# Optimization experiments

Measured on AMD Instinct MI355X. Metric: run time of the kernel, lower is better.

The kernel has to match this reference:

```python
import jax, jax.numpy as jnp
import numpy as np


def setup_inputs() -> dict:
    key = jax.random.key(0)
    k1, k2 = jax.random.split(key)
    S_src, S_tgt, B, H = 2048, 2048, 16, 256
    out_e = jax.random.normal(k1, (S_src, B, 2 * H), dtype=jnp.float32)
    out_d = jax.random.normal(k2, (S_tgt, B, H), dtype=jnp.float32)
    return {"out_e": out_e, "out_d": out_d}


def reference(out_e, out_d):
    # out_e: [S_src, B, 2*H] (bidirectional), out_d: [S_tgt, B, H]
    S, B, H2 = out_e.shape
    # sum the two directions: [S, B, H]
    enc = out_e.reshape(S, B, 2, H2 // 2).sum(axis=2)
    enc = enc.transpose(1, 0, 2)   # [B, S_src, H]
    dec = out_d.transpose(1, 0, 2)  # [B, S_tgt, H]
    # attn scores [B, S_src, S_tgt]; softmax over source positions (dim=1)
    attn = jnp.einsum('bsh,bth->bst', enc, dec)
    attn = jax.nn.softmax(attn, axis=1)
    # context: weighted sum over source positions -> [B, S_tgt, H]
    context = jnp.einsum('bst,bsh->bth', attn, enc)
    return context.transpose(1, 0, 2)  # [S_tgt, B, H]
```

## Files before the change

kernel.cpp:

```cpp
#include <hip/hip_runtime.h>
#include <stdint.h>
#include <stddef.h>

#define BATCH 16
#define SEQ 2048
#define HDIM 256
#define SCHUNK 32
#define TTILE 128
#define NCHUNK 64
#define TILE_U16 8192
#define NTILES 1024
#define PREBLK 2048
#define KSTRIDE 260

typedef float f32x4 __attribute__((ext_vector_type(4)));
typedef float f32x16 __attribute__((ext_vector_type(16)));
typedef _Float16 f16x8 __attribute__((ext_vector_type(8)));
typedef __bf16 bf16x8 __attribute__((ext_vector_type(8)));
typedef unsigned short u16;
typedef u16 u16x8 __attribute__((ext_vector_type(8)));
typedef unsigned int u32;
typedef u32 u32x4 __attribute__((ext_vector_type(4)));
typedef const __attribute__((address_space(1))) u32* gp1_t;
typedef __attribute__((address_space(3))) u32* lp3_t;

static __device__ __forceinline__ u16 f2bf(float f) {
  union { float f; unsigned int u; } v; v.f = f;
  unsigned int u = v.u;
  unsigned int r = u + 0x7FFFu + ((u >> 16) & 1u);
  return (u16)(r >> 16);
}

__global__ __launch_bounds__(256, 8)
void prepass_kernel(const float* __restrict__ e,
                    u16* __restrict__ KH, u16* __restrict__ VT) {
  __shared__ float Ks[16 * KSTRIDE];
  const int tid = threadIdx.x;
  const int bid = blockIdx.x;
  const int h2  = bid & 1;
  const int tb  = bid >> 1;
  const int b   = tb >> 6;
  const int ck  = tb & 63;
  const size_t tile = (size_t)tb * TILE_U16;
  const int r0 = h2 * 16;

  {
    int row = tid >> 4;
    int c16 = tid & 15;
    const float* src = e + ((size_t)(ck * SCHUNK + r0 + row) * BATCH + b) * (2 * HDIM);
#pragma unroll
    for (int u = 0; u < 4; ++u) {
      int col = c16 * 4 + 64 * u;
      float4 xa = *(const float4*)(src + col);
      float4 xb = *(const float4*)(src + col + HDIM);
      float4 s; s.x = xa.x + xb.x; s.y = xa.y + xb.y; s.z = xa.z + xb.z; s.w = xa.w + xb.w;
      *(float4*)&Ks[row * KSTRIDE + col] = s;
    }
  }
  __syncthreads();

  const int lane = tid & 63;
  const int w = tid >> 6;

  {
    int half = lane >> 5;
    int l5   = lane & 31;
    int lm   = l5 & 15;
    int g    = (l5 >> 4) & 1;
#pragma unroll
    for (int i = 0; i < 2; ++i) {
      int kb = w * 4 + i * 2 + half;
      const float* rp = &Ks[lm * KSTRIDE + kb * 16 + g * 8];
      u16x8 hi;
#pragma unroll
      for (int j = 0; j < 8; ++j)
        hi[j] = __builtin_bit_cast(u16, (_Float16)rp[j]);
      int lane_out = g * 32 + r0 + lm;
      *(u16x8*)&KH[tile + (size_t)(kb * 64 + lane_out) * 8] = hi;
    }
  }

  {
    int m = lane & 31;
    int g = lane >> 5;
#pragma unroll
    for (int i = 0; i < 2; ++i) {
      int ht = w * 2 + i;
      int fr = ht * 2 + h2;
      u16x8 v;
#pragma unroll
      for (int j = 0; j < 8; ++j)
        v[j] = f2bf(Ks[(g * 8 + j) * KSTRIDE + ht * 32 + m]);
      *(u16x8*)&VT[tile + (size_t)(fr * 64 + lane) * 8] = v;
    }
  }
}

__global__ __launch_bounds__(512, 2)
void attn_main_kernel(const u16* __restrict__ KH, const u16* __restrict__ VT,
                      const float* __restrict__ dq,
                      float* __restrict__ out) {
  __shared__ alignas(16) u16 KHs[4][TILE_U16];
  __shared__ alignas(16) u16 VTs[6][TILE_U16];

  const int tid  = threadIdx.x;
  const int lane = tid & 63;
  const int wv   = tid >> 6;
  const int wq   = wv & 3;
  const int grp  = wv >> 2;
  const int m    = lane & 31;
  const int g    = lane >> 5;

  const int bid = blockIdx.x;
  const int b  = ((bid & 7) << 1) | ((bid >> 3) & 1);
  const int t0 = (bid >> 4) * TTILE;

  const int tq = t0 + wq * 32 + m;
  const float* qp = dq + ((size_t)tq * BATCH + b) * HDIM;
  f16x8 qh[16];
#pragma unroll
  for (int kb = 0; kb < 16; ++kb) {
    int h = kb * 16 + g * 8;
    float4 f0 = *(const float4*)(qp + h);
    float4 f1 = *(const float4*)(qp + h + 4);
    float xs[8] = {f0.x, f0.y, f0.z, f0.w, f1.x, f1.y, f1.z, f1.w};
    u16x8 hb;
#pragma unroll
    for (int j = 0; j < 8; ++j)
      hb[j] = __builtin_bit_cast(u16, (_Float16)xs[j]);
    qh[kb] = __builtin_bit_cast(f16x8, hb);
  }

  f32x16 ctx[8];
#pragma unroll
  for (int ht = 0; ht < 8; ++ht) ctx[ht] = (f32x16)(0.0f);
  float dsum = 0.0f;
  bf16x8 pa0 = {}, pa1 = {};

  const bool isVT  = (wv >> 1) & 1;
  const int  choff = wv >> 2;
  const int  subbase = (wv & 1) * 8;
  const u16* srcArr = isVT ? VT : KH;
  auto stage = [&](int p) {
    int ckk = 2 * p + choff;
    int ktile = 2 * (p & 1) + choff;
    int vtile = (p % 3) * 2 + choff;
    size_t tb = ((size_t)b * NCHUNK + ckk) * TILE_U16;
    u16* dst = isVT ? &VTs[vtile][0] : &KHs[ktile][0];
#pragma unroll
    for (int i = 0; i < 8; ++i) {
      int sub = subbase + i;
      __builtin_amdgcn_global_load_lds(
          (gp1_t)(const void*)&srcArr[tb + (size_t)sub * 512 + lane * 8],
          (lp3_t)(void*)&dst[sub * 512], 16, 0, 0);
    }
  };

  auto qk = [&](int p, f32x16& a0, f32x16& a1) {
    int kt = 2 * (p & 1) + grp;
#pragma unroll
    for (int kb = 0; kb < 16; kb += 2) {
      f16x8 k0 = __builtin_bit_cast(f16x8, *(const u16x8*)&KHs[kt][kb * 512 + lane * 8]);
      f16x8 k1 = __builtin_bit_cast(f16x8, *(const u16x8*)&KHs[kt][(kb + 1) * 512 + lane * 8]);
      a0 = __builtin_amdgcn_mfma_f32_32x32x16_f16(k0, qh[kb], a0, 0, 0, 0);
      a1 = __builtin_amdgcn_mfma_f32_32x32x16_f16(k1, qh[kb + 1], a1, 0, 0, 0);
    }
  };

  auto pv = [&](int p) {
    int vt_ = (p % 3) * 2 + grp;
#pragma unroll
    for (int ht = 0; ht < 8; ++ht) {
      bf16x8 v0 = __builtin_bit_cast(bf16x8, *(const u16x8*)&VTs[vt_][(ht * 2) * 512 + lane * 8]);
      bf16x8 v1 = __builtin_bit_cast(bf16x8, *(const u16x8*)&VTs[vt_][(ht * 2 + 1) * 512 + lane * 8]);
      ctx[ht] = __builtin_amdgcn_mfma_f32_32x32x16_bf16(pa0, v0, ctx[ht], 0, 0, 0);
      ctx[ht] = __builtin_amdgcn_mfma_f32_32x32x16_bf16(pa1, v1, ctx[ht], 0, 0, 0);
    }
  };

  auto softmax_pack = [&](const f32x16& a0, const f32x16& a1) {
    float pf[16];
#pragma unroll
    for (int r = 0; r < 16; ++r) {
      pf[r] = __expf(a0[r] + a1[r] - 128.0f);
      dsum += pf[r];
    }
    u32 c[8];
#pragma unroll
    for (int q = 0; q < 8; ++q)
      asm("v_cvt_pk_bf16_f32 %0, %1, %2"
          : "=v"(c[q]) : "v"(pf[2 * q]), "v"(pf[2 * q + 1]));
    asm("v_permlane32_swap_b32 %0, %1" : "+v"(c[0]), "+v"(c[2]));
    asm("v_permlane32_swap_b32 %0, %1" : "+v"(c[1]), "+v"(c[3]));
    asm("v_permlane32_swap_b32 %0, %1" : "+v"(c[4]), "+v"(c[6]));
    asm("v_permlane32_swap_b32 %0, %1" : "+v"(c[5]), "+v"(c[7]));
    u32x4 w0 = {c[0], c[1], c[2], c[3]};
    u32x4 w1 = {c[4], c[5], c[6], c[7]};
    pa0 = __builtin_bit_cast(bf16x8, w0);
    pa1 = __builtin_bit_cast(bf16x8, w1);
  };

  stage(0);
  stage(1);
  asm volatile("s_waitcnt vmcnt(8)" ::: "memory");
  __builtin_amdgcn_s_barrier();
  {
    f32x16 a0 = (f32x16)(0.0f), a1 = (f32x16)(0.0f);
    qk(0, a0, a1);
    softmax_pack(a0, a1);
  }

  for (int j = 0; j < 32; ++j) {
    asm volatile("s_waitcnt vmcnt(0)" ::: "memory");
    __builtin_amdgcn_s_barrier();
    if (j < 30) stage(j + 2);

    f32x16 a0 = (f32x16)(0.0f), a1 = (f32x16)(0.0f);
    __builtin_amdgcn_s_setprio(1);
    if (j < 31) qk(j + 1, a0, a1);
    pv(j);
    __builtin_amdgcn_s_setprio(0);
    if (j < 31) softmax_pack(a0, a1);
  }

  dsum += __shfl_xor(dsum, 32, 64);
  __syncthreads();

  float* exch = (wq == 0) ? (float*)&KHs[0][0]
              : (wq == 1) ? (float*)&KHs[2][0]
              : (wq == 2) ? (float*)&VTs[0][0]
                          : (float*)&VTs[2][0];
  float* dex = (float*)&VTs[4][0];

  if (grp == 1) {
#pragma unroll
    for (int r4 = 0; r4 < 4; ++r4)
#pragma unroll
      for (int ht = 0; ht < 8; ++ht) {
        f32x4 v = {ctx[ht][r4 * 4], ctx[ht][r4 * 4 + 1],
                   ctx[ht][r4 * 4 + 2], ctx[ht][r4 * 4 + 3]};
        *(f32x4*)&exch[r4 * 2048 + ht * 256 + lane * 4] = v;
      }
    dex[wq * 64 + lane] = dsum;
  }
  __syncthreads();

  if (grp == 0) {
    float dB = dex[wq * 64 + lane];
    float inv = 1.0f / (dsum + dB);
#pragma unroll
    for (int r4 = 0; r4 < 4; ++r4)
#pragma unroll
      for (int ht = 0; ht < 8; ++ht) {
        f32x4 v = *(const f32x4*)&exch[r4 * 2048 + ht * 256 + lane * 4];
        ctx[ht][r4 * 4]     += v[0];
        ctx[ht][r4 * 4 + 1] += v[1];
        ctx[ht][r4 * 4 + 2] += v[2];
        ctx[ht][r4 * 4 + 3] += v[3];
      }
#pragma unroll
    for (int r = 0; r < 16; ++r) {
      int tl = (r & 3) + 8 * (r >> 2) + 4 * g;
      float rinv = __shfl(inv, tl, 64);
      int t = t0 + wq * 32 + tl;
      float* op = out + ((size_t)t * BATCH + b) * HDIM + m;
#pragma unroll
      for (int ht = 0; ht < 8; ++ht)
        op[ht * 32] = ctx[ht][r] * rinv;
    }
  }
}

extern "C" void kernel_launch(void* const* d_in, const int* in_sizes, int n_in,
                              void* d_out, int out_size, void* d_ws, size_t ws_size,
                              hipStream_t stream) {
  const float* e  = (const float*)d_in[0];
  const float* dq = (const float*)d_in[1];
  float* out = (float*)d_out;
  u16* KH = (u16*)d_ws;
  u16* VT = KH + (size_t)NTILES * TILE_U16;
  prepass_kernel<<<dim3(PREBLK), dim3(256), 0, stream>>>(e, KH, VT);
  attn_main_kernel<<<dim3(BATCH * (SEQ / TTILE)), dim3(512), 0, stream>>>(
      KH, VT, dq, out);
}
```

Measured before the change: 200.8 us.

## Load V tiles directly from global into registers instead of staging in LDS

Removes the six-slot LDS ring for V tiles. Each wave now loads its V fragments straight from global memory into registers, software-pipelined two steps ahead inside the PV MFMA loop. Only K tiles stay staged in LDS, and the staging work is spread over all eight waves. This cuts LDS use a lot, which may allow more blocks per CU and removes LDS write/read traffic for V. The cost is global-load latency on the PV path, since each V tile is now read separately by waves of different blocks. The context reduction is split into two phases so it fits the smaller shared buffer.

```diff
diff --git a/kernel.cpp b/kernel.cpp
--- a/kernel.cpp
+++ b/kernel.cpp
@@ -101,7 +101,7 @@
                       const float* __restrict__ dq,
                       float* __restrict__ out) {
   __shared__ alignas(16) u16 KHs[4][TILE_U16];
-  __shared__ alignas(16) u16 VTs[6][TILE_U16];
+  __shared__ float dex[256];
 
   const int tid  = threadIdx.x;
   const int lane = tid & 63;
@@ -137,21 +137,16 @@
   float dsum = 0.0f;
   bf16x8 pa0 = {}, pa1 = {};
 
-  const bool isVT  = (wv >> 1) & 1;
-  const int  choff = wv >> 2;
-  const int  subbase = (wv & 1) * 8;
-  const u16* srcArr = isVT ? VT : KH;
   auto stage = [&](int p) {
-    int ckk = 2 * p + choff;
-    int ktile = 2 * (p & 1) + choff;
-    int vtile = (p % 3) * 2 + choff;
-    size_t tb = ((size_t)b * NCHUNK + ckk) * TILE_U16;
-    u16* dst = isVT ? &VTs[vtile][0] : &KHs[ktile][0];
-#pragma unroll
-    for (int i = 0; i < 8; ++i) {
-      int sub = subbase + i;
+    int ck2   = 2 * p + (wv >> 2);
+    int ktile = 2 * (p & 1) + (wv >> 2);
+    size_t tb = ((size_t)b * NCHUNK + ck2) * TILE_U16;
+    u16* dst = &KHs[ktile][0];
+#pragma unroll
+    for (int i = 0; i < 4; ++i) {
+      int sub = (wv & 3) * 4 + i;
       __builtin_amdgcn_global_load_lds(
-          (gp1_t)(const void*)&srcArr[tb + (size_t)sub * 512 + lane * 8],
+          (gp1_t)(const void*)&KH[tb + (size_t)sub * 512 + lane * 8],
           (lp3_t)(void*)&dst[sub * 512], 16, 0, 0);
     }
   };
@@ -164,17 +159,6 @@
       f16x8 k1 = __builtin_bit_cast(f16x8, *(const u16x8*)&KHs[kt][(kb + 1) * 512 + lane * 8]);
       a0 = __builtin_amdgcn_mfma_f32_32x32x16_f16(k0, qh[kb], a0, 0, 0, 0);
       a1 = __builtin_amdgcn_mfma_f32_32x32x16_f16(k1, qh[kb + 1], a1, 0, 0, 0);
-    }
-  };
-
-  auto pv = [&](int p) {
-    int vt_ = (p % 3) * 2 + grp;
-#pragma unroll
-    for (int ht = 0; ht < 8; ++ht) {
-      bf16x8 v0 = __builtin_bit_cast(bf16x8, *(const u16x8*)&VTs[vt_][(ht * 2) * 512 + lane * 8]);
-      bf16x8 v1 = __builtin_bit_cast(bf16x8, *(const u16x8*)&VTs[vt_][(ht * 2 + 1) * 512 + lane * 8]);
-      ctx[ht] = __builtin_amdgcn_mfma_f32_32x32x16_bf16(pa0, v0, ctx[ht], 0, 0, 0);
-      ctx[ht] = __builtin_amdgcn_mfma_f32_32x32x16_bf16(pa1, v1, ctx[ht], 0, 0, 0);
     }
   };
 
@@ -202,7 +186,7 @@
 
   stage(0);
   stage(1);
-  asm volatile("s_waitcnt vmcnt(8)" ::: "memory");
+  asm volatile("s_waitcnt vmcnt(4)" ::: "memory");
   __builtin_amdgcn_s_barrier();
   {
     f32x16 a0 = (f32x16)(0.0f), a1 = (f32x16)(0.0f);
@@ -213,61 +197,89 @@
   for (int j = 0; j < 32; ++j) {
     asm volatile("s_waitcnt vmcnt(0)" ::: "memory");
     __builtin_amdgcn_s_barrier();
+
+    const int ckk = 2 * j + grp;
+    const u16* vb = VT + ((size_t)b * NCHUNK + ckk) * TILE_U16;
+
+    u16x8 vv0[8], vv1[8];
+    vv0[0] = *(const u16x8*)&vb[(size_t)(0 * 64 + lane) * 8];
+    vv1[0] = *(const u16x8*)&vb[(size_t)(1 * 64 + lane) * 8];
+    vv0[1] = *(const u16x8*)&vb[(size_t)(2 * 64 + lane) * 8];
+    vv1[1] = *(const u16x8*)&vb[(size_t)(3 * 64 + lane) * 8];
+
     if (j < 30) stage(j + 2);
 
     f32x16 a0 = (f32x16)(0.0f), a1 = (f32x16)(0.0f);
     __builtin_amdgcn_s_setprio(1);
     if (j < 31) qk(j + 1, a0, a1);
-    pv(j);
+
+#pragma unroll
+    for (int ht = 0; ht < 8; ++ht) {
+      if (ht < 6) {
+        vv0[ht + 2] = *(const u16x8*)&vb[(size_t)((2 * ht + 4) * 64 + lane) * 8];
+        vv1[ht + 2] = *(const u16x8*)&vb[(size_t)((2 * ht + 5) * 64 + lane) * 8];
+      }
+      bf16x8 v0 = __builtin_bit_cast(bf16x8, vv0[ht]);
+      bf16x8 v1 = __builtin_bit_cast(bf16x8, vv1[ht]);
+      ctx[ht] = __builtin_amdgcn_mfma_f32_32x32x16_bf16(pa0, v0, ctx[ht], 0, 0, 0);
+      ctx[ht] = __builtin_amdgcn_mfma_f32_32x32x16_bf16(pa1, v1, ctx[ht], 0, 0, 0);
+    }
     __builtin_amdgcn_s_setprio(0);
+
     if (j < 31) softmax_pack(a0, a1);
   }
 
   dsum += __shfl_xor(dsum, 32, 64);
   __syncthreads();
 
-  float* exch = (wq == 0) ? (float*)&KHs[0][0]
-              : (wq == 1) ? (float*)&KHs[2][0]
-              : (wq == 2) ? (float*)&VTs[0][0]
-                          : (float*)&VTs[2][0];
-  float* dex = (float*)&VTs[4][0];
-
-  if (grp == 1) {
-#pragma unroll
-    for (int r4 = 0; r4 < 4; ++r4)
-#pragma unroll
-      for (int ht = 0; ht < 8; ++ht) {
-        f32x4 v = {ctx[ht][r4 * 4], ctx[ht][r4 * 4 + 1],
-                   ctx[ht][r4 * 4 + 2], ctx[ht][r4 * 4 + 3]};
-        *(f32x4*)&exch[r4 * 2048 + ht * 256 + lane * 4] = v;
+  float* exch = (float*)&KHs[0][0] + wq * 4096;
+  float inv = 0.0f;
+
+#pragma unroll
+  for (int ph = 0; ph < 2; ++ph) {
+    if (grp == 1) {
+#pragma unroll
+      for (int r4 = 0; r4 < 4; ++r4)
+#pragma unroll
+        for (int hh = 0; hh < 4; ++hh) {
+          int ht = ph * 4 + hh;
+          f32x4 v = {ctx[ht][r4 * 4], ctx[ht][r4 * 4 + 1],
+                     ctx[ht][r4 * 4 + 2], ctx[ht][r4 * 4 + 3]};
+          *(f32x4*)&exch[r4 * 1024 + hh * 256 + lane * 4] = v;
+        }
+      if (ph == 0) dex[wq * 64 + lane] = dsum;
+    }
+    __syncthreads();
+    if (grp == 0) {
+      if (ph == 0) {
+        float dB = dex[wq * 64 + lane];
+        inv = 1.0f / (dsum + dB);
       }
-    dex[wq * 64 + lane] = dsum;
-  }
-  __syncthreads();
-
-  if (grp == 0) {
-    float dB = dex[wq * 64 + lane];
-    float inv = 1.0f / (dsum + dB);
-#pragma unroll
-    for (int r4 = 0; r4 < 4; ++r4)
-#pragma unroll
-      for (int ht = 0; ht < 8; ++ht) {
-        f32x4 v = *(const f32x4*)&exch[r4 * 2048 + ht * 256 + lane * 4];
-        ctx[ht][r4 * 4]     += v[0];
-        ctx[ht][r4 * 4 + 1] += v[1];
-        ctx[ht][r4 * 4 + 2] += v[2];
-        ctx[ht][r4 * 4 + 3] += v[3];
+#pragma unroll
+      for (int r4 = 0; r4 < 4; ++r4)
+#pragma unroll
+        for (int hh = 0; hh < 4; ++hh) {
+          int ht = ph * 4 + hh;
+          f32x4 v = *(const f32x4*)&exch[r4 * 1024 + hh * 256 + lane * 4];
+          ctx[ht][r4 * 4]     += v[0];
+          ctx[ht][r4 * 4 + 1] += v[1];
+          ctx[ht][r4 * 4 + 2] += v[2];
+          ctx[ht][r4 * 4 + 3] += v[3];
+        }
+#pragma unroll
+      for (int r = 0; r < 16; ++r) {
+        int tl = (r & 3) + 8 * (r >> 2) + 4 * g;
+        float rinv = __shfl(inv, tl, 64);
+        int t = t0 + wq * 32 + tl;
+        float* op = out + ((size_t)t * BATCH + b) * HDIM + m;
+#pragma unroll
+        for (int hh = 0; hh < 4; ++hh) {
+          int ht = ph * 4 + hh;
+          op[ht * 32] = ctx[ht][r] * rinv;
+        }
       }
-#pragma unroll
-    for (int r = 0; r < 16; ++r) {
-      int tl = (r & 3) + 8 * (r >> 2) + 4 * g;
-      float rinv = __shfl(inv, tl, 64);
-      int t = t0 + wq * 32 + tl;
-      float* op = out + ((size_t)t * BATCH + b) * HDIM + m;
-#pragma unroll
-      for (int ht = 0; ht < 8; ++ht)
-        op[ht * 32] = ctx[ht][r] * rinv;
-    }
+    }
+    __syncthreads();
   }
 }
 
```

Result: slower. 298.8 us (+48.8%).

## Split source chunks across blocks with atomic reduction instead of intra-block wave groups

Applied to the files above, without the earlier changes.

Replaces the 512-thread block, whose two wave groups split the source chunks and reduce through LDS, with 256-thread blocks that each handle half the source range. This doubles the grid, halves LDS use per block and should allow more resident blocks. Partial context and denominators are combined with global float atomicAdds into the zeroed output and a global denominator array, then a separate divide kernel normalises. The cost is two extra kernel launches, an extra pass over the output, atomic traffic, and a summation order that is no longer deterministic.

```diff
diff --git a/kernel.cpp b/kernel.cpp
--- a/kernel.cpp
+++ b/kernel.cpp
@@ -24,11 +24,21 @@
 typedef const __attribute__((address_space(1))) u32* gp1_t;
 typedef __attribute__((address_space(3))) u32* lp3_t;
 
+__device__ alignas(16) float g_den[SEQ * BATCH];
+
 static __device__ __forceinline__ u16 f2bf(float f) {
   union { float f; unsigned int u; } v; v.f = f;
   unsigned int u = v.u;
   unsigned int r = u + 0x7FFFu + ((u >> 16) & 1u);
   return (u16)(r >> 16);
+}
+
+__global__ __launch_bounds__(256, 8)
+void zero_kernel(float* __restrict__ out) {
+  int idx = blockIdx.x * 256 + threadIdx.x;
+  ((f32x4*)out)[idx] = (f32x4)(0.0f);
+  if (blockIdx.x < 32)
+    ((f32x4*)g_den)[blockIdx.x * 256 + threadIdx.x] = (f32x4)(0.0f);
 }
 
 __global__ __launch_bounds__(256, 8)
@@ -96,24 +106,23 @@
   }
 }
 
-__global__ __launch_bounds__(512, 2)
+__global__ __launch_bounds__(256, 2)
 void attn_main_kernel(const u16* __restrict__ KH, const u16* __restrict__ VT,
                       const float* __restrict__ dq,
                       float* __restrict__ out) {
-  __shared__ alignas(16) u16 KHs[4][TILE_U16];
-  __shared__ alignas(16) u16 VTs[6][TILE_U16];
+  __shared__ alignas(16) u16 KHs[2][TILE_U16];
+  __shared__ alignas(16) u16 VTs[3][TILE_U16];
 
   const int tid  = threadIdx.x;
   const int lane = tid & 63;
-  const int wv   = tid >> 6;
-  const int wq   = wv & 3;
-  const int grp  = wv >> 2;
+  const int wq   = tid >> 6;
   const int m    = lane & 31;
   const int g    = lane >> 5;
 
   const int bid = blockIdx.x;
   const int b  = ((bid & 7) << 1) | ((bid >> 3) & 1);
-  const int t0 = (bid >> 4) * TTILE;
+  const int t0 = ((bid >> 4) & 15) * TTILE;
+  const int c0 = ((bid >> 8) & 1) * 32;
 
   const int tq = t0 + wq * 32 + m;
   const float* qp = dq + ((size_t)tq * BATCH + b) * HDIM;
@@ -137,16 +146,12 @@
   float dsum = 0.0f;
   bf16x8 pa0 = {}, pa1 = {};
 
-  const bool isVT  = (wv >> 1) & 1;
-  const int  choff = wv >> 2;
-  const int  subbase = (wv & 1) * 8;
-  const u16* srcArr = isVT ? VT : KH;
-  auto stage = [&](int p) {
-    int ckk = 2 * p + choff;
-    int ktile = 2 * (p & 1) + choff;
-    int vtile = (p % 3) * 2 + choff;
-    size_t tb = ((size_t)b * NCHUNK + ckk) * TILE_U16;
-    u16* dst = isVT ? &VTs[vtile][0] : &KHs[ktile][0];
+  const u16* srcArr = (wq < 2) ? KH : VT;
+  const int  subbase = (wq & 1) * 8;
+  auto stage = [&](int c) {
+    int kset = c & 1, vset = c % 3;
+    size_t tb = ((size_t)b * NCHUNK + c0 + c) * TILE_U16;
+    u16* dst = (wq < 2) ? &KHs[kset][0] : &VTs[vset][0];
 #pragma unroll
     for (int i = 0; i < 8; ++i) {
       int sub = subbase + i;
@@ -156,8 +161,8 @@
     }
   };
 
-  auto qk = [&](int p, f32x16& a0, f32x16& a1) {
-    int kt = 2 * (p & 1) + grp;
+  auto qk = [&](int c, f32x16& a0, f32x16& a1) {
+    int kt = c & 1;
 #pragma unroll
     for (int kb = 0; kb < 16; kb += 2) {
       f16x8 k0 = __builtin_bit_cast(f16x8, *(const u16x8*)&KHs[kt][kb * 512 + lane * 8]);
@@ -167,8 +172,8 @@
     }
   };
 
-  auto pv = [&](int p) {
-    int vt_ = (p % 3) * 2 + grp;
+  auto pv = [&](int c) {
+    int vt_ = c % 3;
 #pragma unroll
     for (int ht = 0; ht < 8; ++ht) {
       bf16x8 v0 = __builtin_bit_cast(bf16x8, *(const u16x8*)&VTs[vt_][(ht * 2) * 512 + lane * 8]);
@@ -210,65 +215,40 @@
     softmax_pack(a0, a1);
   }
 
-  for (int j = 0; j < 32; ++j) {
+  for (int c = 0; c < 32; ++c) {
     asm volatile("s_waitcnt vmcnt(0)" ::: "memory");
     __builtin_amdgcn_s_barrier();
-    if (j < 30) stage(j + 2);
+    if (c < 30) stage(c + 2);
 
     f32x16 a0 = (f32x16)(0.0f), a1 = (f32x16)(0.0f);
     __builtin_amdgcn_s_setprio(1);
-    if (j < 31) qk(j + 1, a0, a1);
-    pv(j);
+    if (c < 31) qk(c + 1, a0, a1);
+    pv(c);
     __builtin_amdgcn_s_setprio(0);
-    if (j < 31) softmax_pack(a0, a1);
+    if (c < 31) softmax_pack(a0, a1);
   }
 
   dsum += __shfl_xor(dsum, 32, 64);
-  __syncthreads();
-
-  float* exch = (wq == 0) ? (float*)&KHs[0][0]
-              : (wq == 1) ? (float*)&KHs[2][0]
-              : (wq == 2) ? (float*)&VTs[0][0]
-                          : (float*)&VTs[2][0];
-  float* dex = (float*)&VTs[4][0];
-
-  if (grp == 1) {
-#pragma unroll
-    for (int r4 = 0; r4 < 4; ++r4)
-#pragma unroll
-      for (int ht = 0; ht < 8; ++ht) {
-        f32x4 v = {ctx[ht][r4 * 4], ctx[ht][r4 * 4 + 1],
-                   ctx[ht][r4 * 4 + 2], ctx[ht][r4 * 4 + 3]};
-        *(f32x4*)&exch[r4 * 2048 + ht * 256 + lane * 4] = v;
-      }
-    dex[wq * 64 + lane] = dsum;
-  }
-  __syncthreads();
-
-  if (grp == 0) {
-    float dB = dex[wq * 64 + lane];
-    float inv = 1.0f / (dsum + dB);
-#pragma unroll
-    for (int r4 = 0; r4 < 4; ++r4)
-#pragma unroll
-      for (int ht = 0; ht < 8; ++ht) {
-        f32x4 v = *(const f32x4*)&exch[r4 * 2048 + ht * 256 + lane * 4];
-        ctx[ht][r4 * 4]     += v[0];
-        ctx[ht][r4 * 4 + 1] += v[1];
-        ctx[ht][r4 * 4 + 2] += v[2];
-        ctx[ht][r4 * 4 + 3] += v[3];
-      }
-#pragma unroll
-    for (int r = 0; r < 16; ++r) {
-      int tl = (r & 3) + 8 * (r >> 2) + 4 * g;
-      float rinv = __shfl(inv, tl, 64);
-      int t = t0 + wq * 32 + tl;
-      float* op = out + ((size_t)t * BATCH + b) * HDIM + m;
-#pragma unroll
-      for (int ht = 0; ht < 8; ++ht)
-        op[ht * 32] = ctx[ht][r] * rinv;
-    }
-  }
+  if (lane < 32)
+    atomicAdd(&g_den[(size_t)(t0 + wq * 32 + lane) * BATCH + b], dsum);
+#pragma unroll
+  for (int r = 0; r < 16; ++r) {
+    int tl = (r & 3) + 8 * (r >> 2) + 4 * g;
+    int t = t0 + wq * 32 + tl;
+    float* op = out + ((size_t)t * BATCH + b) * HDIM + m;
+#pragma unroll
+    for (int ht = 0; ht < 8; ++ht)
+      atomicAdd(op + ht * 32, ctx[ht][r]);
+  }
+}
+
+__global__ __launch_bounds__(256, 8)
+void divide_kernel(float* __restrict__ out) {
+  int idx = blockIdx.x * 256 + threadIdx.x;
+  f32x4 v = ((f32x4*)out)[idx];
+  float inv = 1.0f / g_den[idx >> 6];
+  v[0] *= inv; v[1] *= inv; v[2] *= inv; v[3] *= inv;
+  ((f32x4*)out)[idx] = v;
 }
 
 extern "C" void kernel_launch(void* const* d_in, const int* in_sizes, int n_in,
@@ -279,7 +259,10 @@
   float* out = (float*)d_out;
   u16* KH = (u16*)d_ws;
   u16* VT = KH + (size_t)NTILES * TILE_U16;
+
+  zero_kernel<<<dim3(SEQ * BATCH * HDIM / 4 / 256), dim3(256), 0, stream>>>(out);
   prepass_kernel<<<dim3(PREBLK), dim3(256), 0, stream>>>(e, KH, VT);
-  attn_main_kernel<<<dim3(BATCH * (SEQ / TTILE)), dim3(512), 0, stream>>>(
+  attn_main_kernel<<<dim3(BATCH * (SEQ / TTILE) * 2), dim3(256), 0, stream>>>(
       KH, VT, dq, out);
-}
+  divide_kernel<<<dim3(SEQ * BATCH * HDIM / 4 / 256), dim3(256), 0, stream>>>(out);
+}
```

New measurement: 263.6 us. 1.31x slower.
